# Kernel tuning notes

Hardware: AMD Instinct MI355X
Metric: run time of the kernel (lower is better)

The kernel has to match this reference:

```python
import jax, jax.numpy as jnp
import numpy as np

B, C_IN, C_OUT, N, MODES, TEMB = 16, 64, 64, 16384, 2048, 512


def setup_inputs() -> dict:
    key = jax.random.key(0)
    k1, k2, k3, k4, k5 = jax.random.split(key, 5)
    scale = 1.0 / (C_IN * C_OUT)
    return {
        "x": jax.random.normal(k1, (B, C_IN, N), dtype=jnp.float32),
        "temb": jax.random.normal(k2, (B, TEMB), dtype=jnp.float32),
        "wr": jax.random.normal(k3, (C_IN, C_OUT, MODES), dtype=jnp.float32) * scale,
        "wi": jax.random.normal(k4, (C_IN, C_OUT, MODES), dtype=jnp.float32) * scale,
        "dense_w": jax.random.normal(k5, (C_IN, TEMB), dtype=jnp.float32) * (1.0 / np.sqrt(TEMB)),
        "dense_b": jnp.zeros((C_IN,), dtype=jnp.float32),
    }


def reference(x, temb, wr, wi, dense_w, dense_b):
    # x: [B, C_in, N] real signal; spectral conv in Fourier space (FNO)
    b, c_in, n = x.shape
    modes = wr.shape[-1]
    x_ft = jnp.fft.rfft(x, axis=-1)  # [B, C_in, N//2+1] complex
    # temb injection: Dense_0(act(temb))[:, :, None], act = SiLU (DDPM-style)
    t = jax.nn.silu(temb) @ dense_w.T + dense_b  # [B, C_in]
    xm = x_ft[..., :modes] + t[:, :, None].astype(x_ft.dtype)
    w = wr + 1j * wi  # [C_in, C_out, modes]
    # contract_dense eq for order-3 input: 'abc,bdc->adc'
    out_m = jnp.einsum("bim,iom->bom", xm, w)  # [B, C_out, modes]
    c_out = w.shape[1]
    out_ft = jnp.zeros((b, c_out, n // 2 + 1), dtype=out_m.dtype)
    out_ft = out_ft.at[..., :modes].set(out_m)
    return jnp.fft.irfft(out_ft, n=n, axis=-1)  # [B, C_out, N]
```

## Files before the change

### kernel.cpp

```cpp
#include <hip/hip_runtime.h>
#include <math.h>

#define NB    16
#define CIN   64
#define COUT  64
#define NN    16384
#define HH    8192
#define MODES 2048
#define TEMBD 512

__device__ __forceinline__ int swz(int e) { return e ^ ((e >> 5) & 31); }
__device__ __forceinline__ int rev13(int x) { return (int)(__brev((unsigned)x) >> 19); }

__device__ __forceinline__ void gl_lds16(const void* gsrc, void* lds) {
  __builtin_amdgcn_global_load_lds(
      (const __attribute__((address_space(1))) void*)gsrc,
      (__attribute__((address_space(3))) void*)lds, 16, 0, 0);
}

__global__ void init_tw_k(float2* __restrict__ tw8, float2* __restrict__ tw16) {
  int j = blockIdx.x * blockDim.x + threadIdx.x;
  if (j < 4096) {
    double a = (2.0 * 3.14159265358979323846 / 8192.0) * (double)j;
    tw8[j] = make_float2((float)cos(a), (float)sin(a));
  }
  if (j < 2048) {
    double a = (2.0 * 3.14159265358979323846 / 16384.0) * (double)j;
    tw16[j] = make_float2((float)cos(a), (float)sin(a));
  }
}

template<int J, int S, int LH_HI>
__device__ __forceinline__ void pass_dif(float* zr, float* zi, int pbase,
                                         const float2* __restrict__ tw) {
  int lh = LH_HI;
#pragma unroll
  for (int half = J / 2; half >= 1; half >>= 1, --lh) {
#pragma unroll
    for (int blk = 0; blk < J; blk += 2 * half) {
#pragma unroll
      for (int q = 0; q < half; ++q) {
        const int j0 = blk + q, j1 = j0 + half;
        const float2 w = tw[(pbase + q * S) << (12 - lh)];
        const float ur = zr[j0], ui = zi[j0];
        const float vr = zr[j1], vi = zi[j1];
        zr[j0] = ur + vr; zi[j0] = ui + vi;
        const float br = ur - vr, bi = ui - vi;
        zr[j1] = br * w.x + bi * w.y;
        zi[j1] = bi * w.x - br * w.y;
      }
    }
  }
}

template<int J, int S, int LH_LO>
__device__ __forceinline__ void pass_dit(float* zr, float* zi, int pbase,
                                         const float2* __restrict__ tw) {
  int lh = LH_LO;
#pragma unroll
  for (int half = 1; half <= J / 2; half <<= 1, ++lh) {
#pragma unroll
    for (int blk = 0; blk < J; blk += 2 * half) {
#pragma unroll
      for (int q = 0; q < half; ++q) {
        const int j0 = blk + q, j1 = j0 + half;
        const float2 w = tw[(pbase + q * S) << (12 - lh)];
        const float vr = zr[j1], vi = zi[j1];
        const float tr = vr * w.x - vi * w.y;
        const float ti = vr * w.y + vi * w.x;
        const float ur = zr[j0], ui = zi[j0];
        zr[j0] = ur + tr; zi[j0] = ui + ti;
        zr[j1] = ur - tr; zi[j1] = ui - ti;
      }
    }
  }
}

__global__ __launch_bounds__(256) void fwd_fft_k(
    const float* __restrict__ x, const float* __restrict__ temb,
    const float* __restrict__ dw, const float* __restrict__ db,
    const float2* __restrict__ tw8, const float2* __restrict__ tw16,
    float2* __restrict__ xm)
{
  __shared__ float re[HH];
  __shared__ float im[HH];
  const int row = blockIdx.x;
  const int b = row >> 6, ci = row & 63;
  const int tid = threadIdx.x;

  float part = 0.f;
  {
    const float* tb = temb + b * TEMBD;
    const float* wrow = dw + ci * TEMBD;
    for (int j = tid; j < TEMBD; j += 256) {
      float v = tb[j];
      part += v * wrow[j] / (1.f + __expf(-v));
    }
    for (int off = 32; off > 0; off >>= 1) part += __shfl_down(part, off, 64);
    if ((tid & 63) == 0) re[tid >> 6] = part;
  }
  __syncthreads();
  const float tval = re[0] + re[1] + re[2] + re[3] + db[ci];
  __syncthreads();

  float zr[32], zi[32];

  const float2* xr = (const float2*)(x + (size_t)row * NN);
#pragma unroll
  for (int g = 0; g < 2; ++g) {
    const int i0 = tid + g * 256;
#pragma unroll
    for (int j = 0; j < 16; ++j) {
      float2 v = xr[i0 + j * 512];
      zr[g * 16 + j] = v.x; zi[g * 16 + j] = v.y;
    }
  }
#pragma unroll
  for (int g = 0; g < 2; ++g) {
    const int i0 = tid + g * 256;
    pass_dif<16, 512, 12>(zr + g * 16, zi + g * 16, i0, tw8);
#pragma unroll
    for (int j = 0; j < 16; ++j) {
      const int e = swz(i0 + j * 512);
      re[e] = zr[g * 16 + j]; im[e] = zi[g * 16 + j];
    }
  }
  __syncthreads();

  {
    const int r = tid & 31;
#pragma unroll
    for (int g = 0; g < 2; ++g) {
      const int base = ((tid >> 5) + g * 8) * 512 + r;
#pragma unroll
      for (int j = 0; j < 16; ++j) {
        const int e = swz(base + j * 32);
        zr[g * 16 + j] = re[e]; zi[g * 16 + j] = im[e];
      }
      pass_dif<16, 32, 8>(zr + g * 16, zi + g * 16, r, tw8);
#pragma unroll
      for (int j = 0; j < 16; ++j) {
        const int e = swz(base + j * 32);
        re[e] = zr[g * 16 + j]; im[e] = zi[g * 16 + j];
      }
    }
  }
  __syncthreads();

  {
    const int base = tid * 32;
#pragma unroll
    for (int j = 0; j < 32; ++j) {
      const int e = swz(base + j);
      zr[j] = re[e]; zi[j] = im[e];
    }
    pass_dif<32, 1, 4>(zr, zi, 0, tw8);
#pragma unroll
    for (int j = 0; j < 32; ++j) {
      if ((j & 3) == 1 || (j & 3) == 2) continue;
      const int e = swz(base + j);
      re[e] = zr[j]; im[e] = zi[j];
    }
  }
  __syncthreads();

  float2* xrow = xm + (size_t)row * MODES;
  for (int k = tid; k < MODES; k += 256) {
    const int ka = swz(rev13(k));
    const int kb = swz(rev13((HH - k) & (HH - 1)));
    float Ar = re[ka], Ai = im[ka];
    float Br = re[kb], Bi = -im[kb];
    float Sr = 0.5f * (Ar + Br), Si = 0.5f * (Ai + Bi);
    float Dr = 0.5f * (Ar - Br), Di = 0.5f * (Ai - Bi);
    float2 wv = tw16[k];
    float c = wv.x, s = wv.y;
    float Xr = Sr - s * Dr + c * Di;
    float Xi = Si - s * Di - c * Dr;
    xrow[k] = make_float2(Xr + tval, Xi);
  }
}

__global__ __launch_bounds__(256) void spec_mul_k(
    const float2* __restrict__ xm, const float* __restrict__ wr,
    const float* __restrict__ wi, float2* __restrict__ om)
{
  __shared__ float2 xs[128 * 16];
  __shared__ float2 wsr[8 * 16 * 4];
  __shared__ float2 wsi[8 * 16 * 4];

  const int tid = threadIdx.x;
  const int mm = tid & 15;
  const int og = (tid >> 4) & 3;
  const int h  = tid >> 6;
  const int ln = tid & 63;

  const int m0 = blockIdx.x * 16;
  const int o0 = blockIdx.y * 8;

  float2 acc[4][2];
#pragma unroll
  for (int j = 0; j < 4; ++j) {
    acc[j][0] = make_float2(0.f, 0.f);
    acc[j][1] = make_float2(0.f, 0.f);
  }

  for (int ic = 0; ic < 8; ++ic) {
#pragma unroll
    for (int t = 0; t < 4; ++t) {
      const int r = h * 32 + t * 8 + (ln >> 3);
      const int b = r >> 3, il = r & 7;
      const float2* src =
          xm + ((size_t)(b * CIN + ic * 8 + il)) * MODES + m0 + (ln & 7) * 2;
      gl_lds16((const void*)src, (void*)((char*)xs + (h * 32 + t * 8) * 128));
    }
#pragma unroll
    for (int t = 0; t < 2; ++t) {
      const int f = tid + t * 256;
      const int fm = f & 15, fg = (f >> 4) & 3, fil = f >> 6;
      const size_t rA =
          ((size_t)((ic * 8 + fil) * COUT + o0 + fg * 2)) * MODES + m0 + fm;
      const size_t rB = rA + MODES;
      wsr[(fil * 16 + fm) * 4 + fg] = make_float2(wr[rA], wr[rB]);
      wsi[(fil * 16 + fm) * 4 + fg] = make_float2(wi[rA], wi[rB]);
    }
    __syncthreads();

#pragma unroll
    for (int il = 0; il < 8; ++il) {
      const float2 wrp = wsr[(il * 16 + mm) * 4 + og];
      const float2 wip = wsi[(il * 16 + mm) * 4 + og];
#pragma unroll
      for (int j = 0; j < 4; ++j) {
        const float2 xv = xs[((h * 4 + j) * 8 + il) * 16 + mm];
        acc[j][0].x += xv.x * wrp.x - xv.y * wip.x;
        acc[j][0].y += xv.x * wip.x + xv.y * wrp.x;
        acc[j][1].x += xv.x * wrp.y - xv.y * wip.y;
        acc[j][1].y += xv.x * wip.y + xv.y * wrp.y;
      }
    }
    if (ic < 7) __syncthreads();
  }

#pragma unroll
  for (int j = 0; j < 4; ++j) {
    const int b = h * 4 + j;
    const size_t ob = ((size_t)(b * COUT + o0 + og * 2)) * MODES + m0 + mm;
    om[ob] = acc[j][0];
    om[ob + MODES] = acc[j][1];
  }
}

__global__ __launch_bounds__(256) void inv_fft_k(
    const float2* __restrict__ om, const float2* __restrict__ tw8,
    const float2* __restrict__ tw16, float* __restrict__ out)
{
  __shared__ float re[HH];
  __shared__ float im[HH];
  const int row = blockIdx.x;
  const int tid = threadIdx.x;

  for (int q = tid; q < HH; q += 256) { re[q] = 0.f; im[q] = 0.f; }
  __syncthreads();

  const float2* grow = om + (size_t)row * MODES;
  for (int k = tid; k < MODES; k += 256) {
    float2 g = grow[k];
    if (k == 0) {
      float v = 0.5f * g.x;
      re[0] = v; im[0] = v;
    } else {
      float2 wv = tw16[k];
      float Pr = 0.5f * g.x, Pi = 0.5f * g.y;
      float c = wv.x, s = wv.y;
      float sr = -(c * Pi + s * Pr);
      float si =  (c * Pr - s * Pi);
      int ka = swz(rev13(k));
      int kb = swz(rev13(HH - k));
      re[ka] = Pr + sr; im[ka] = Pi + si;
      re[kb] = Pr - sr; im[kb] = -(Pi - si);
    }
  }
  __syncthreads();

  float zr[32], zi[32];

  {
    const int base = tid * 32;
#pragma unroll
    for (int j = 0; j < 32; ++j) {
      const int e = swz(base + j);
      zr[j] = re[e]; zi[j] = im[e];
    }
    pass_dit<32, 1, 0>(zr, zi, 0, tw8);
#pragma unroll
    for (int j = 0; j < 32; ++j) {
      const int e = swz(base + j);
      re[e] = zr[j]; im[e] = zi[j];
    }
  }
  __syncthreads();

  {
    const int r = tid & 31;
#pragma unroll
    for (int g = 0; g < 2; ++g) {
      const int base = ((tid >> 5) + g * 8) * 512 + r;
#pragma unroll
      for (int j = 0; j < 16; ++j) {
        const int e = swz(base + j * 32);
        zr[g * 16 + j] = re[e]; zi[g * 16 + j] = im[e];
      }
      pass_dit<16, 32, 5>(zr + g * 16, zi + g * 16, r, tw8);
#pragma unroll
      for (int j = 0; j < 16; ++j) {
        const int e = swz(base + j * 32);
        re[e] = zr[g * 16 + j]; im[e] = zi[g * 16 + j];
      }
    }
  }
  __syncthreads();

  {
    float2* orow = (float2*)(out + (size_t)row * NN);
    const float sc = 1.0f / 8192.0f;
#pragma unroll
    for (int g = 0; g < 2; ++g) {
      const int i0 = tid + g * 256;
#pragma unroll
      for (int j = 0; j < 16; ++j) {
        const int e = swz(i0 + j * 512);
        zr[g * 16 + j] = re[e]; zi[g * 16 + j] = im[e];
      }
      pass_dit<16, 512, 9>(zr + g * 16, zi + g * 16, i0, tw8);
#pragma unroll
      for (int j = 0; j < 16; ++j) {
        orow[i0 + j * 512] = make_float2(zr[g * 16 + j] * sc, zi[g * 16 + j] * sc);
      }
    }
  }
}

extern "C" void kernel_launch(void* const* d_in, const int* in_sizes, int n_in,
                              void* d_out, int out_size, void* d_ws, size_t ws_size,
                              hipStream_t stream) {
  const float* x    = (const float*)d_in[0];
  const float* temb = (const float*)d_in[1];
  const float* wr   = (const float*)d_in[2];
  const float* wi   = (const float*)d_in[3];
  const float* dw   = (const float*)d_in[4];
  const float* db   = (const float*)d_in[5];
  float* out = (float*)d_out;

  char* ws = (char*)d_ws;
  float2* tw8  = (float2*)ws;
  float2* tw16 = (float2*)(ws + 32768);
  float2* xm   = (float2*)(ws + 65536);
  float2* om   = (float2*)(ws + 65536 + (size_t)16777216);

  hipLaunchKernelGGL(init_tw_k, dim3(16), dim3(256), 0, stream, tw8, tw16);
  hipLaunchKernelGGL(fwd_fft_k, dim3(NB * CIN), dim3(256), 0, stream,
                     x, temb, dw, db, tw8, tw16, xm);
  hipLaunchKernelGGL(spec_mul_k, dim3(MODES / 16, COUT / 8), dim3(256), 0, stream,
                     xm, wr, wi, om);
  hipLaunchKernelGGL(inv_fft_k, dim3(NB * COUT), dim3(256), 0, stream,
                     om, tw8, tw16, out);
}
```

Measured before the change: 254.5 us.

## Double-buffer x and register-prefetch weights in spectral multiply kernel

The spectral multiply kernel now keeps two LDS buffers for the x tile and issues async global-to-LDS loads for the next input-channel chunk while computing on the current one. Weights for the next chunk are prefetched into registers and written to LDS after compute. The thread-to-(mode, output group) mapping is also swapped so og varies fastest, which changes the LDS weight access pattern. This hides global load latency at the cost of extra LDS, extra registers and an additional barrier per iteration.

After: 243.5 us. -4.3%, faster.

```diff
diff --git a/kernel.cpp b/kernel.cpp
--- a/kernel.cpp
+++ b/kernel.cpp
@@ -184,13 +184,13 @@
     const float2* __restrict__ xm, const float* __restrict__ wr,
     const float* __restrict__ wi, float2* __restrict__ om)
 {
-  __shared__ float2 xs[128 * 16];
+  __shared__ float2 xs[2][128 * 16];
   __shared__ float2 wsr[8 * 16 * 4];
   __shared__ float2 wsi[8 * 16 * 4];
 
   const int tid = threadIdx.x;
-  const int mm = tid & 15;
-  const int og = (tid >> 4) & 3;
+  const int og = tid & 3;
+  const int mm = (tid >> 2) & 15;
   const int h  = tid >> 6;
   const int ln = tid & 63;
 
@@ -204,42 +204,78 @@
     acc[j][1] = make_float2(0.f, 0.f);
   }
 
-  for (int ic = 0; ic < 8; ++ic) {
-#pragma unroll
-    for (int t = 0; t < 4; ++t) {
-      const int r = h * 32 + t * 8 + (ln >> 3);
-      const int b = r >> 3, il = r & 7;
-      const float2* src =
-          xm + ((size_t)(b * CIN + ic * 8 + il)) * MODES + m0 + (ln & 7) * 2;
-      gl_lds16((const void*)src, (void*)((char*)xs + (h * 32 + t * 8) * 128));
-    }
-#pragma unroll
-    for (int t = 0; t < 2; ++t) {
-      const int f = tid + t * 256;
-      const int fm = f & 15, fg = (f >> 4) & 3, fil = f >> 6;
-      const size_t rA =
-          ((size_t)((ic * 8 + fil) * COUT + o0 + fg * 2)) * MODES + m0 + fm;
-      const size_t rB = rA + MODES;
-      wsr[(fil * 16 + fm) * 4 + fg] = make_float2(wr[rA], wr[rB]);
-      wsi[(fil * 16 + fm) * 4 + fg] = make_float2(wi[rA], wi[rB]);
-    }
+  float2 pr[2], pi[2];
+
+#define STAGE_X(ic, buf)                                                      \
+  {                                                                           \
+    _Pragma("unroll")                                                         \
+    for (int t = 0; t < 4; ++t) {                                             \
+      const int r = h * 32 + t * 8 + (ln >> 3);                               \
+      const int b = r >> 3, il = r & 7;                                       \
+      const float2* src =                                                     \
+          xm + ((size_t)(b * CIN + (ic) * 8 + il)) * MODES + m0 + (ln & 7) * 2;\
+      gl_lds16((const void*)src,                                              \
+               (void*)((char*)&xs[buf][0] + (h * 32 + t * 8) * 128));         \
+    }                                                                         \
+  }
+
+#define W_LOAD(ic)                                                            \
+  {                                                                           \
+    _Pragma("unroll")                                                         \
+    for (int t = 0; t < 2; ++t) {                                             \
+      const int f = tid + t * 256;                                            \
+      const int fm = f & 15, fg = (f >> 4) & 3, fil = f >> 6;                 \
+      const size_t rA =                                                       \
+          ((size_t)(((ic) * 8 + fil) * COUT + o0 + fg * 2)) * MODES + m0 + fm;\
+      pr[t] = make_float2(wr[rA], wr[rA + MODES]);                            \
+      pi[t] = make_float2(wi[rA], wi[rA + MODES]);                            \
+    }                                                                         \
+  }
+
+#define W_WRITE()                                                             \
+  {                                                                           \
+    _Pragma("unroll")                                                         \
+    for (int t = 0; t < 2; ++t) {                                             \
+      const int f = tid + t * 256;                                            \
+      const int fm = f & 15, fg = (f >> 4) & 3, fil = f >> 6;                 \
+      wsr[(fil * 16 + fm) * 4 + fg] = pr[t];                                  \
+      wsi[(fil * 16 + fm) * 4 + fg] = pi[t];                                  \
+    }                                                                         \
+  }
+
+#define COMPUTE(buf)                                                          \
+  {                                                                           \
+    _Pragma("unroll")                                                         \
+    for (int il = 0; il < 8; ++il) {                                          \
+      const float2 wrp = wsr[(il * 16 + mm) * 4 + og];                        \
+      const float2 wip = wsi[(il * 16 + mm) * 4 + og];                        \
+      _Pragma("unroll")                                                       \
+      for (int j = 0; j < 4; ++j) {                                           \
+        const float2 xv = xs[buf][((h * 4 + j) * 8 + il) * 16 + mm];          \
+        acc[j][0].x += xv.x * wrp.x - xv.y * wip.x;                           \
+        acc[j][0].y += xv.x * wip.x + xv.y * wrp.x;                           \
+        acc[j][1].x += xv.x * wrp.y - xv.y * wip.y;                           \
+        acc[j][1].y += xv.x * wip.y + xv.y * wrp.y;                           \
+      }                                                                       \
+    }                                                                         \
+  }
+
+  STAGE_X(0, 0);
+  W_LOAD(0);
+  W_WRITE();
+  __syncthreads();
+
+#pragma unroll 1
+  for (int ic = 0; ic < 7; ++ic) {
+    const int buf = ic & 1;
+    STAGE_X(ic + 1, buf ^ 1);
+    W_LOAD(ic + 1);
+    COMPUTE(buf);
     __syncthreads();
-
-#pragma unroll
-    for (int il = 0; il < 8; ++il) {
-      const float2 wrp = wsr[(il * 16 + mm) * 4 + og];
-      const float2 wip = wsi[(il * 16 + mm) * 4 + og];
-#pragma unroll
-      for (int j = 0; j < 4; ++j) {
-        const float2 xv = xs[((h * 4 + j) * 8 + il) * 16 + mm];
-        acc[j][0].x += xv.x * wrp.x - xv.y * wip.x;
-        acc[j][0].y += xv.x * wip.x + xv.y * wrp.x;
-        acc[j][1].x += xv.x * wrp.y - xv.y * wip.y;
-        acc[j][1].y += xv.x * wip.y + xv.y * wrp.y;
-      }
-    }
-    if (ic < 7) __syncthreads();
-  }
+    W_WRITE();
+    __syncthreads();
+  }
+  COMPUTE(1);
 
 #pragma unroll
   for (int j = 0; j < 4; ++j) {
@@ -248,6 +284,10 @@
     om[ob] = acc[j][0];
     om[ob + MODES] = acc[j][1];
   }
+#undef STAGE_X
+#undef W_LOAD
+#undef W_WRITE
+#undef COMPUTE
 }
 
 __global__ __launch_bounds__(256) void inv_fft_k(
```
